# Performance work log

Measured on AMD Instinct MI355X. Metric: run time of the kernel, lower is better.

## Reference

```python
import jax, jax.numpy as jnp
import numpy as np

B = 32768        # graphs
NODES = 8        # nodes per graph (512 / 64)
N = B * NODES    # total nodes = 262144
K = 4            # Chebyshev order


def setup_inputs() -> dict:
    key = jax.random.key(0)
    ks = jax.random.split(key, 10)
    # block-diagonal fully-connected graphs (no self loops): 56 directed edges/graph
    s, d = np.nonzero(~np.eye(NODES, dtype=bool))
    offs = np.arange(B, dtype=np.int64)[:, None] * NODES
    edge_src = jnp.asarray((s[None, :] + offs).reshape(-1))
    edge_dst = jnp.asarray((d[None, :] + offs).reshape(-1))
    E = edge_src.shape[0]
    x = jax.random.normal(ks[0], (N, 8), dtype=jnp.float32)
    edge_weight = jax.random.uniform(ks[1], (E,), dtype=jnp.float32, minval=0.1, maxval=1.0)
    sc = 0.2
    return {
        'x': x, 'edge_src': edge_src, 'edge_dst': edge_dst, 'edge_weight': edge_weight,
        'w1': jax.random.normal(ks[2], (K, 8, 16), jnp.float32) * sc,  'b1': jnp.zeros((16,), jnp.float32),
        'w2': jax.random.normal(ks[3], (K, 16, 32), jnp.float32) * sc, 'b2': jnp.zeros((32,), jnp.float32),
        'w3': jax.random.normal(ks[4], (K, 32, 64), jnp.float32) * sc, 'b3': jnp.zeros((64,), jnp.float32),
        'fc1_w': jax.random.normal(ks[5], (512, 256), jnp.float32) * 0.04, 'fc1_b': jnp.zeros((256,), jnp.float32),
        'fc2_w': jax.random.normal(ks[6], (256, 128), jnp.float32) * 0.06, 'fc2_b': jnp.zeros((128,), jnp.float32),
        'fc3_w': jax.random.normal(ks[7], (128, 5), jnp.float32) * 0.09,   'fc3_b': jnp.zeros((5,), jnp.float32),
        'num_graphs': B,
    }


def _cheb(x, W, b, norm_w, edge_src, edge_dst):
    # PyG ChebConv: Tx_0 = x, Tx_1 = L_hat x, Tx_k = 2 L_hat Tx_{k-1} - Tx_{k-2}
    n = x.shape[0]
    def prop(t):  # L_hat @ t  (zero diagonal, off-diag = -D^-1/2 A D^-1/2)
        return jax.ops.segment_sum(norm_w[:, None] * t[edge_src], edge_dst, num_segments=n)
    out = x @ W[0]
    Tx0, Tx1 = x, prop(x)
    out = out + Tx1 @ W[1]
    for k in range(2, W.shape[0]):
        Tx2 = 2.0 * prop(Tx1) - Tx0
        out = out + Tx2 @ W[k]
        Tx0, Tx1 = Tx1, Tx2
    return out + b


def reference(x, edge_src, edge_dst, edge_weight, w1, b1, w2, b2, w3, b3,
              fc1_w, fc1_b, fc2_w, fc2_b, fc3_w, fc3_b, num_graphs):
    n = x.shape[0]
    # sym-normalized scaled Laplacian weights (lambda_max = 2.0)
    deg = jax.ops.segment_sum(edge_weight, edge_src, num_segments=n)
    dis = jnp.where(deg > 0, jax.lax.rsqrt(deg), 0.0)
    norm_w = -dis[edge_src] * edge_weight * dis[edge_dst]
    h = jax.nn.relu(_cheb(x, w1, b1, norm_w, edge_src, edge_dst))
    h = jax.nn.relu(_cheb(h, w2, b2, norm_w, edge_src, edge_dst))
    h = jax.nn.relu(_cheb(h, w3, b3, norm_w, edge_src, edge_dst))
    h = h.reshape(num_graphs, -1)               # (B, 512)
    h = jax.nn.relu(h @ fc1_w + fc1_b)           # dropout inactive in eval
    h = jax.nn.relu(h @ fc2_w + fc2_b)
    logits = h @ fc3_w + fc3_b
    return jax.nn.log_softmax(logits, axis=1)
```

## Files before the change

kernel.cpp:

```cpp
#include <hip/hip_runtime.h>
#include <hip/hip_bf16.h>
#include <math.h>

#define NGRAPH 32768

typedef __attribute__((ext_vector_type(8))) short short8;
typedef __attribute__((ext_vector_type(4))) float f32x4;

__device__ inline short f2bf(float f) {
    __hip_bfloat16 h = __float2bfloat16(f);
    return *reinterpret_cast<short*>(&h);
}

struct __align__(16) WaveScratch {
    float L[8][8];
    float dis[8];
    float Tt[2][32][8];
};

template<int CIN>
__device__ inline void props3(WaveScratch& S, short (*At)[136], int wid, int lane) {
    const int n = lane & 7, cb0 = lane >> 3;
#pragma unroll
    for (int k = 1; k <= 3; ++k) {
        const int pp = (k + 1) & 1;
#pragma unroll
        for (int i = 0; i < CIN / 8; ++i) {
            const int c = cb0 + 8 * i;
            float4 l0 = *(const float4*)&S.L[n][0];
            float4 l1 = *(const float4*)&S.L[n][4];
            float4 t0 = *(const float4*)&S.Tt[pp][c][0];
            float4 t1 = *(const float4*)&S.Tt[pp][c][4];
            float s = l0.x * t0.x;
            s = fmaf(l0.y, t0.y, s); s = fmaf(l0.z, t0.z, s); s = fmaf(l0.w, t0.w, s);
            s = fmaf(l1.x, t1.x, s); s = fmaf(l1.y, t1.y, s);
            s = fmaf(l1.z, t1.z, s); s = fmaf(l1.w, t1.w, s);
            float v = (k == 1) ? s : fmaf(2.f, s, -S.Tt[pp ^ 1][c][n]);
            S.Tt[pp ^ 1][c][n] = v;
            At[wid * 8 + n][k * CIN + c] = f2bf(v);
        }
    }
}

__device__ inline short8 load_bfrag(const float* __restrict__ W, int COUT, int co, int kb) {
    short8 r;
#pragma unroll
    for (int j = 0; j < 8; ++j) r[j] = f2bf(W[(size_t)(kb + j) * COUT + co]);
    return r;
}

__global__ __launch_bounds__(256, 3) void cheb_fused(
    const float* __restrict__ x,
    const float* __restrict__ ew,
    const float* __restrict__ w1, const float* __restrict__ b1,
    const float* __restrict__ w2, const float* __restrict__ b2,
    const float* __restrict__ w3, const float* __restrict__ b3,
    __hip_bfloat16* __restrict__ h3)
{
    __shared__ WaveScratch ws[4];
    __shared__ short At[32][136];
    __shared__ float sB1[16], sB2[32], sB3[64];

    const int t = threadIdx.x;
    const int wid = t >> 6, lane = t & 63;
    const int fr = lane & 15;
    const int kk = (lane >> 4) * 8;
    const int q  = lane >> 4;

    if (t < 16) sB1[t] = b1[t];
    if (t < 32) sB2[t] = b2[t];
    if (t < 64) sB3[t] = b3[t];

    short8 W1f = {};
    if (wid < 2) W1f = load_bfrag(w1, 16, fr, kk);
    short8 W2f[2];
    {
        const int nt = wid & 1;
#pragma unroll
        for (int s = 0; s < 2; ++s) W2f[s] = load_bfrag(w2, 32, nt * 16 + fr, s * 32 + kk);
    }
    short8 W3f[2][4];
    {
        const int nt0 = (wid & 1) * 2;
#pragma unroll
        for (int tt = 0; tt < 2; ++tt)
#pragma unroll
            for (int s = 0; s < 4; ++s)
                W3f[tt][s] = load_bfrag(w3, 64, (nt0 + tt) * 16 + fr, s * 32 + kk);
    }

    const int g = blockIdx.x * 4 + wid;
    WaveScratch& S = ws[wid];

    if (lane < 8) {
        const float* e = ew + (size_t)g * 56 + lane * 7;
        float d = 0.f;
#pragma unroll
        for (int j = 0; j < 7; ++j) d += e[j];
        S.dis[lane] = rsqrtf(d);
    }
    {
        float xv = x[(size_t)g * 64 + lane];
        int n = lane >> 3, c = lane & 7;
        S.Tt[0][c][n] = xv;
        At[wid * 8 + n][c] = f2bf(xv);
    }
    if (lane < 56) {
        int s = lane / 7, j = lane % 7;
        int d = j + (j >= s ? 1 : 0);
        float w = ew[(size_t)g * 56 + lane];
        S.L[d][s] = -S.dis[s] * w * S.dis[d];
    } else if (lane < 64) {
        S.L[lane - 56][lane - 56] = 0.f;
    }

    props3<8>(S, At, wid, lane);
    __syncthreads();
    if (wid < 2) {
        const int mt = wid;
        f32x4 acc = {};
        short8 a = *(const short8*)&At[mt * 16 + fr][kk];
        acc = __builtin_amdgcn_mfma_f32_16x16x32_bf16(a, W1f, acc, 0, 0, 0);
        float vr[4];
#pragma unroll
        for (int r = 0; r < 4; ++r) vr[r] = fmaxf(acc[r] + sB1[fr], 0.f);
        *(float4*)&ws[mt * 2 + (q >> 1)].Tt[0][fr][(q & 1) * 4] =
            float4{vr[0], vr[1], vr[2], vr[3]};
#pragma unroll
        for (int r = 0; r < 4; ++r) At[mt * 16 + q * 4 + r][fr] = f2bf(vr[r]);
    }
    __syncthreads();

    props3<16>(S, At, wid, lane);
    __syncthreads();
    {
        const int mt = wid >> 1, nt = wid & 1;
        f32x4 acc = {};
#pragma unroll
        for (int s = 0; s < 2; ++s) {
            short8 a = *(const short8*)&At[mt * 16 + fr][s * 32 + kk];
            acc = __builtin_amdgcn_mfma_f32_16x16x32_bf16(a, W2f[s], acc, 0, 0, 0);
        }
        const int col = nt * 16 + fr;
        float vr[4];
#pragma unroll
        for (int r = 0; r < 4; ++r) vr[r] = fmaxf(acc[r] + sB2[col], 0.f);
        *(float4*)&ws[mt * 2 + (q >> 1)].Tt[0][col][(q & 1) * 4] =
            float4{vr[0], vr[1], vr[2], vr[3]};
#pragma unroll
        for (int r = 0; r < 4; ++r) At[mt * 16 + q * 4 + r][col] = f2bf(vr[r]);
    }
    __syncthreads();

    props3<32>(S, At, wid, lane);
    __syncthreads();
    {
        const int mt = wid >> 1, nt0 = (wid & 1) * 2;
        f32x4 acc0 = {}, acc1 = {};
#pragma unroll
        for (int s = 0; s < 4; ++s) {
            short8 a = *(const short8*)&At[mt * 16 + fr][s * 32 + kk];
            acc0 = __builtin_amdgcn_mfma_f32_16x16x32_bf16(a, W3f[0][s], acc0, 0, 0, 0);
            acc1 = __builtin_amdgcn_mfma_f32_16x16x32_bf16(a, W3f[1][s], acc1, 0, 0, 0);
        }
        const int gbase = blockIdx.x * 4;
        const int c0 = nt0 * 16 + fr;
#pragma unroll
        for (int r = 0; r < 4; ++r) {
            int R = mt * 16 + q * 4 + r;
            size_t base = (size_t)(gbase + (R >> 3)) * 512 + (R & 7) * 64;
            h3[base + c0]      = __float2bfloat16(fmaxf(acc0[r] + sB3[c0], 0.f));
            h3[base + c0 + 16] = __float2bfloat16(fmaxf(acc1[r] + sB3[c0 + 16], 0.f));
        }
    }
}

__global__ __launch_bounds__(256) void transpose_cast(
    const float* __restrict__ W, __hip_bfloat16* __restrict__ Wt, int K, int N)
{
    __shared__ float tile[32][33];
    const int kb = blockIdx.x * 32, nb = blockIdx.y * 32;
    const int tx = threadIdx.x % 32, ty = threadIdx.x / 32;
    for (int i = ty; i < 32; i += 8)
        tile[i][tx] = W[(size_t)(kb + i) * N + nb + tx];
    __syncthreads();
    for (int i = ty; i < 32; i += 8)
        Wt[(size_t)(nb + i) * K + kb + tx] = __float2bfloat16(tile[tx][i]);
}

template<bool OUT_BF16>
__global__ __launch_bounds__(256) void mfma_fc(
    const __hip_bfloat16* __restrict__ A, const __hip_bfloat16* __restrict__ Bt,
    const float* __restrict__ bias, void* __restrict__ Cout, int M, int N, int K)
{
    __shared__ short As[128][40];
    __shared__ short Bs[128][40];
    const int t = threadIdx.x;
    const int wid = t >> 6, lane = t & 63;
    const int m0 = blockIdx.x * 128, n0 = blockIdx.y * 128;
    const int wm = (wid >> 1) * 64, wn = (wid & 1) * 64;

    const int r_row = t >> 1;
    const int r_k   = (t & 1) * 16;

    const int fr = lane & 15;
    const int kk = (lane >> 4) * 8;

    f32x4 acc[4][4] = {};

    for (int k0 = 0; k0 < K; k0 += 32) {
        short8 av0 = *(const short8*)&A [(size_t)(m0 + r_row) * K + k0 + r_k];
        short8 av1 = *(const short8*)&A [(size_t)(m0 + r_row) * K + k0 + r_k + 8];
        short8 bv0 = *(const short8*)&Bt[(size_t)(n0 + r_row) * K + k0 + r_k];
        short8 bv1 = *(const short8*)&Bt[(size_t)(n0 + r_row) * K + k0 + r_k + 8];
        __syncthreads();
        *(short8*)&As[r_row][r_k]     = av0;
        *(short8*)&As[r_row][r_k + 8] = av1;
        *(short8*)&Bs[r_row][r_k]     = bv0;
        *(short8*)&Bs[r_row][r_k + 8] = bv1;
        __syncthreads();

        short8 af[4], bf[4];
#pragma unroll
        for (int fm = 0; fm < 4; ++fm) af[fm] = *(const short8*)&As[wm + fm * 16 + fr][kk];
#pragma unroll
        for (int fn = 0; fn < 4; ++fn) bf[fn] = *(const short8*)&Bs[wn + fn * 16 + fr][kk];
#pragma unroll
        for (int fm = 0; fm < 4; ++fm)
#pragma unroll
            for (int fn = 0; fn < 4; ++fn)
                acc[fm][fn] = __builtin_amdgcn_mfma_f32_16x16x32_bf16(
                    af[fm], bf[fn], acc[fm][fn], 0, 0, 0);
    }

    const int orow = (lane >> 4) * 4;
#pragma unroll
    for (int fm = 0; fm < 4; ++fm) {
#pragma unroll
        for (int fn = 0; fn < 4; ++fn) {
            const int n = n0 + wn + fn * 16 + fr;
            const float bn = bias[n];
#pragma unroll
            for (int r = 0; r < 4; ++r) {
                const int m = m0 + wm + fm * 16 + orow + r;
                float v = fmaxf(acc[fm][fn][r] + bn, 0.f);
                if (OUT_BF16)
                    ((__hip_bfloat16*)Cout)[(size_t)m * N + n] = __float2bfloat16(v);
                else
                    ((float*)Cout)[(size_t)m * N + n] = v;
            }
        }
    }
}

__global__ __launch_bounds__(256) void fc3_logsoftmax(
    const float* __restrict__ A,
    const float* __restrict__ W,
    const float* __restrict__ b,
    float* __restrict__ out,
    int M)
{
    __shared__ float sW[128 * 5];
    __shared__ float sB[5];
    const int t = threadIdx.x;
    for (int i = t; i < 640; i += 256) sW[i] = W[i];
    if (t < 5) sB[t] = b[t];
    __syncthreads();

    int row = blockIdx.x * blockDim.x + t;
    if (row >= M) return;
    float logits[5];
#pragma unroll
    for (int j = 0; j < 5; ++j) logits[j] = sB[j];
    const float* a = A + (size_t)row * 128;
    for (int k = 0; k < 128; k += 4) {
        float4 av = *(const float4*)&a[k];
        const float* wk = sW + k * 5;
#pragma unroll
        for (int j = 0; j < 5; ++j) logits[j] = fmaf(av.x, wk[j], logits[j]);
#pragma unroll
        for (int j = 0; j < 5; ++j) logits[j] = fmaf(av.y, wk[5 + j], logits[j]);
#pragma unroll
        for (int j = 0; j < 5; ++j) logits[j] = fmaf(av.z, wk[10 + j], logits[j]);
#pragma unroll
        for (int j = 0; j < 5; ++j) logits[j] = fmaf(av.w, wk[15 + j], logits[j]);
    }
    float mx = logits[0];
#pragma unroll
    for (int j = 1; j < 5; ++j) mx = fmaxf(mx, logits[j]);
    float s = 0.f;
#pragma unroll
    for (int j = 0; j < 5; ++j) s += expf(logits[j] - mx);
    float lse = mx + logf(s);
#pragma unroll
    for (int j = 0; j < 5; ++j) out[(size_t)row * 5 + j] = logits[j] - lse;
}

extern "C" void kernel_launch(void* const* d_in, const int* in_sizes, int n_in,
                              void* d_out, int out_size, void* d_ws, size_t ws_size,
                              hipStream_t stream) {
    const float* x     = (const float*)d_in[0];
    const float* ew    = (const float*)d_in[3];
    const float* w1    = (const float*)d_in[4];
    const float* b1    = (const float*)d_in[5];
    const float* w2    = (const float*)d_in[6];
    const float* b2    = (const float*)d_in[7];
    const float* w3    = (const float*)d_in[8];
    const float* b3    = (const float*)d_in[9];
    const float* fc1_w = (const float*)d_in[10];
    const float* fc1_b = (const float*)d_in[11];
    const float* fc2_w = (const float*)d_in[12];
    const float* fc2_b = (const float*)d_in[13];
    const float* fc3_w = (const float*)d_in[14];
    const float* fc3_b = (const float*)d_in[15];
    float* out = (float*)d_out;

    char* p = (char*)d_ws;
    __hip_bfloat16* h3  = (__hip_bfloat16*)p;                 p += (size_t)NGRAPH * 512 * 2;
    __hip_bfloat16* a1  = (__hip_bfloat16*)p;                 p += (size_t)NGRAPH * 256 * 2;
    float*          a2  = (float*)p;                          p += (size_t)NGRAPH * 128 * 4;
    __hip_bfloat16* Wt1 = (__hip_bfloat16*)p;                 p += (size_t)256 * 512 * 2;
    __hip_bfloat16* Wt2 = (__hip_bfloat16*)p;

    transpose_cast<<<dim3(512 / 32, 256 / 32), 256, 0, stream>>>(fc1_w, Wt1, 512, 256);
    transpose_cast<<<dim3(256 / 32, 128 / 32), 256, 0, stream>>>(fc2_w, Wt2, 256, 128);
    cheb_fused<<<NGRAPH / 4, 256, 0, stream>>>(x, ew, w1, b1, w2, b2, w3, b3, h3);
    mfma_fc<true ><<<dim3(NGRAPH / 128, 256 / 128), 256, 0, stream>>>(h3, Wt1, fc1_b, a1,
                                                                      NGRAPH, 256, 512);
    mfma_fc<false><<<dim3(NGRAPH / 128, 128 / 128), 256, 0, stream>>>(a1, Wt2, fc2_b, a2,
                                                                      NGRAPH, 128, 256);
    fc3_logsoftmax<<<NGRAPH / 256, 256, 0, stream>>>(a2, fc3_w, fc3_b, out, NGRAPH);
}
```

Before: 187.1 us.

## Make Chebyshev layers wave-local, loop two graph pairs per wave, store fc2 as bf16

Each wave now handles two graphs (16 rows) end to end, with its own LDS tile, so the block-wide __syncthreads between the propagation and MFMA stages go away. Each wave holds all W1/W2/W3 fragments and biases in registers, loops twice over graph pairs, and keeps Laplacian rows in registers. Occupancy is lowered to 2 blocks per SM because of the extra register use. Separately, the fc2 output becomes bf16 to halve traffic into the fc3/log-softmax kernel, at some precision cost.

```diff
diff --git a/kernel.cpp b/kernel.cpp
--- a/kernel.cpp
+++ b/kernel.cpp
@@ -11,33 +11,36 @@
     __hip_bfloat16 h = __float2bfloat16(f);
     return *reinterpret_cast<short*>(&h);
 }
-
-struct __align__(16) WaveScratch {
-    float L[8][8];
-    float dis[8];
-    float Tt[2][32][8];
+__device__ inline float bf2f(short u) {
+    unsigned int x = ((unsigned int)(unsigned short)u) << 16;
+    return *reinterpret_cast<float*>(&x);
+}
+
+struct __align__(16) WaveCtx {
+    short At[16][136];
+    float Tt[2][32][16];
+    float L[2][8][8];
+    float dis[2][8];
 };
 
 template<int CIN>
-__device__ inline void props3(WaveScratch& S, short (*At)[136], int wid, int lane) {
-    const int n = lane & 7, cb0 = lane >> 3;
+__device__ inline void props3(WaveCtx& C, float4 Lr0, float4 Lr1,
+                              int pg, int pn, int pcb) {
 #pragma unroll
     for (int k = 1; k <= 3; ++k) {
         const int pp = (k + 1) & 1;
 #pragma unroll
-        for (int i = 0; i < CIN / 8; ++i) {
-            const int c = cb0 + 8 * i;
-            float4 l0 = *(const float4*)&S.L[n][0];
-            float4 l1 = *(const float4*)&S.L[n][4];
-            float4 t0 = *(const float4*)&S.Tt[pp][c][0];
-            float4 t1 = *(const float4*)&S.Tt[pp][c][4];
-            float s = l0.x * t0.x;
-            s = fmaf(l0.y, t0.y, s); s = fmaf(l0.z, t0.z, s); s = fmaf(l0.w, t0.w, s);
-            s = fmaf(l1.x, t1.x, s); s = fmaf(l1.y, t1.y, s);
-            s = fmaf(l1.z, t1.z, s); s = fmaf(l1.w, t1.w, s);
-            float v = (k == 1) ? s : fmaf(2.f, s, -S.Tt[pp ^ 1][c][n]);
-            S.Tt[pp ^ 1][c][n] = v;
-            At[wid * 8 + n][k * CIN + c] = f2bf(v);
+        for (int i = 0; i < CIN / 4; ++i) {
+            const int c = pcb + 4 * i;
+            float4 t0 = *(const float4*)&C.Tt[pp][c][pg * 8];
+            float4 t1 = *(const float4*)&C.Tt[pp][c][pg * 8 + 4];
+            float s = Lr0.x * t0.x;
+            s = fmaf(Lr0.y, t0.y, s); s = fmaf(Lr0.z, t0.z, s); s = fmaf(Lr0.w, t0.w, s);
+            s = fmaf(Lr1.x, t1.x, s); s = fmaf(Lr1.y, t1.y, s);
+            s = fmaf(Lr1.z, t1.z, s); s = fmaf(Lr1.w, t1.w, s);
+            float v = (k == 1) ? s : fmaf(2.f, s, -C.Tt[pp ^ 1][c][pg * 8 + pn]);
+            C.Tt[pp ^ 1][c][pg * 8 + pn] = v;
+            C.At[pg * 8 + pn][k * CIN + c] = f2bf(v);
         }
     }
 }
@@ -49,7 +52,7 @@
     return r;
 }
 
-__global__ __launch_bounds__(256, 3) void cheb_fused(
+__global__ __launch_bounds__(256, 2) void cheb_fused(
     const float* __restrict__ x,
     const float* __restrict__ ew,
     const float* __restrict__ w1, const float* __restrict__ b1,
@@ -57,120 +60,123 @@
     const float* __restrict__ w3, const float* __restrict__ b3,
     __hip_bfloat16* __restrict__ h3)
 {
-    __shared__ WaveScratch ws[4];
-    __shared__ short At[32][136];
-    __shared__ float sB1[16], sB2[32], sB3[64];
+    __shared__ WaveCtx ctx[4];
 
     const int t = threadIdx.x;
     const int wid = t >> 6, lane = t & 63;
     const int fr = lane & 15;
-    const int kk = (lane >> 4) * 8;
     const int q  = lane >> 4;
-
-    if (t < 16) sB1[t] = b1[t];
-    if (t < 32) sB2[t] = b2[t];
-    if (t < 64) sB3[t] = b3[t];
-
-    short8 W1f = {};
-    if (wid < 2) W1f = load_bfrag(w1, 16, fr, kk);
-    short8 W2f[2];
-    {
-        const int nt = wid & 1;
-#pragma unroll
-        for (int s = 0; s < 2; ++s) W2f[s] = load_bfrag(w2, 32, nt * 16 + fr, s * 32 + kk);
-    }
-    short8 W3f[2][4];
-    {
-        const int nt0 = (wid & 1) * 2;
-#pragma unroll
-        for (int tt = 0; tt < 2; ++tt)
-#pragma unroll
-            for (int s = 0; s < 4; ++s)
-                W3f[tt][s] = load_bfrag(w3, 64, (nt0 + tt) * 16 + fr, s * 32 + kk);
-    }
-
-    const int g = blockIdx.x * 4 + wid;
-    WaveScratch& S = ws[wid];
-
-    if (lane < 8) {
-        const float* e = ew + (size_t)g * 56 + lane * 7;
-        float d = 0.f;
-#pragma unroll
-        for (int j = 0; j < 7; ++j) d += e[j];
-        S.dis[lane] = rsqrtf(d);
-    }
-    {
-        float xv = x[(size_t)g * 64 + lane];
-        int n = lane >> 3, c = lane & 7;
-        S.Tt[0][c][n] = xv;
-        At[wid * 8 + n][c] = f2bf(xv);
-    }
-    if (lane < 56) {
-        int s = lane / 7, j = lane % 7;
-        int d = j + (j >= s ? 1 : 0);
-        float w = ew[(size_t)g * 56 + lane];
-        S.L[d][s] = -S.dis[s] * w * S.dis[d];
-    } else if (lane < 64) {
-        S.L[lane - 56][lane - 56] = 0.f;
-    }
-
-    props3<8>(S, At, wid, lane);
-    __syncthreads();
-    if (wid < 2) {
-        const int mt = wid;
-        f32x4 acc = {};
-        short8 a = *(const short8*)&At[mt * 16 + fr][kk];
-        acc = __builtin_amdgcn_mfma_f32_16x16x32_bf16(a, W1f, acc, 0, 0, 0);
-        float vr[4];
-#pragma unroll
-        for (int r = 0; r < 4; ++r) vr[r] = fmaxf(acc[r] + sB1[fr], 0.f);
-        *(float4*)&ws[mt * 2 + (q >> 1)].Tt[0][fr][(q & 1) * 4] =
-            float4{vr[0], vr[1], vr[2], vr[3]};
-#pragma unroll
-        for (int r = 0; r < 4; ++r) At[mt * 16 + q * 4 + r][fr] = f2bf(vr[r]);
-    }
-    __syncthreads();
-
-    props3<16>(S, At, wid, lane);
-    __syncthreads();
-    {
-        const int mt = wid >> 1, nt = wid & 1;
-        f32x4 acc = {};
-#pragma unroll
-        for (int s = 0; s < 2; ++s) {
-            short8 a = *(const short8*)&At[mt * 16 + fr][s * 32 + kk];
-            acc = __builtin_amdgcn_mfma_f32_16x16x32_bf16(a, W2f[s], acc, 0, 0, 0);
-        }
-        const int col = nt * 16 + fr;
-        float vr[4];
-#pragma unroll
-        for (int r = 0; r < 4; ++r) vr[r] = fmaxf(acc[r] + sB2[col], 0.f);
-        *(float4*)&ws[mt * 2 + (q >> 1)].Tt[0][col][(q & 1) * 4] =
-            float4{vr[0], vr[1], vr[2], vr[3]};
-#pragma unroll
-        for (int r = 0; r < 4; ++r) At[mt * 16 + q * 4 + r][col] = f2bf(vr[r]);
-    }
-    __syncthreads();
-
-    props3<32>(S, At, wid, lane);
-    __syncthreads();
-    {
-        const int mt = wid >> 1, nt0 = (wid & 1) * 2;
-        f32x4 acc0 = {}, acc1 = {};
-#pragma unroll
-        for (int s = 0; s < 4; ++s) {
-            short8 a = *(const short8*)&At[mt * 16 + fr][s * 32 + kk];
-            acc0 = __builtin_amdgcn_mfma_f32_16x16x32_bf16(a, W3f[0][s], acc0, 0, 0, 0);
-            acc1 = __builtin_amdgcn_mfma_f32_16x16x32_bf16(a, W3f[1][s], acc1, 0, 0, 0);
-        }
-        const int gbase = blockIdx.x * 4;
-        const int c0 = nt0 * 16 + fr;
-#pragma unroll
-        for (int r = 0; r < 4; ++r) {
-            int R = mt * 16 + q * 4 + r;
-            size_t base = (size_t)(gbase + (R >> 3)) * 512 + (R & 7) * 64;
-            h3[base + c0]      = __float2bfloat16(fmaxf(acc0[r] + sB3[c0], 0.f));
-            h3[base + c0 + 16] = __float2bfloat16(fmaxf(acc1[r] + sB3[c0 + 16], 0.f));
+    const int kk = q * 8;
+    WaveCtx& C = ctx[wid];
+
+    const int pg = lane >> 5, pn = lane & 7, pcb = (lane >> 3) & 3;
+
+    short8 W1f = load_bfrag(w1, 16, fr, kk);
+    short8 W2f[2][2];
+#pragma unroll
+    for (int nt = 0; nt < 2; ++nt)
+#pragma unroll
+        for (int ks = 0; ks < 2; ++ks)
+            W2f[nt][ks] = load_bfrag(w2, 32, nt * 16 + fr, ks * 32 + kk);
+    short8 W3f[4][4];
+#pragma unroll
+    for (int nt = 0; nt < 4; ++nt)
+#pragma unroll
+        for (int ks = 0; ks < 4; ++ks)
+            W3f[nt][ks] = load_bfrag(w3, 64, nt * 16 + fr, ks * 32 + kk);
+    const float b1r = b1[fr];
+    float b2r[2] = {b2[fr], b2[16 + fr]};
+    float b3r[4] = {b3[fr], b3[16 + fr], b3[32 + fr], b3[48 + fr]};
+
+#pragma unroll 1
+    for (int it = 0; it < 2; ++it) {
+        const int g0 = blockIdx.x * 16 + (it * 4 + wid) * 2;
+
+        if (lane < 16) {
+            int g = lane >> 3, n = lane & 7;
+            const float* e = ew + (size_t)(g0 + g) * 56 + n * 7;
+            float d = 0.f;
+#pragma unroll
+            for (int j = 0; j < 7; ++j) d += e[j];
+            C.dis[g][n] = rsqrtf(d);
+        }
+#pragma unroll
+        for (int j = 0; j < 2; ++j) {
+            float xv = x[(size_t)g0 * 64 + j * 64 + lane];
+            int n = lane >> 3, c = lane & 7;
+            C.Tt[0][c][j * 8 + n] = xv;
+            C.At[j * 8 + n][c] = f2bf(xv);
+        }
+#pragma unroll
+        for (int j = 0; j < 2; ++j) {
+            if (lane < 56) {
+                int s = lane / 7, jj = lane % 7;
+                int d = jj + (jj >= s ? 1 : 0);
+                float w = ew[(size_t)(g0 + j) * 56 + lane];
+                C.L[j][d][s] = -C.dis[j][s] * w * C.dis[j][d];
+            } else {
+                C.L[j][lane - 56][lane - 56] = 0.f;
+            }
+        }
+        float4 Lr0 = *(const float4*)&C.L[pg][pn][0];
+        float4 Lr1 = *(const float4*)&C.L[pg][pn][4];
+
+        props3<8>(C, Lr0, Lr1, pg, pn, pcb);
+        {
+            f32x4 acc = {};
+            short8 a = *(const short8*)&C.At[fr][kk];
+            acc = __builtin_amdgcn_mfma_f32_16x16x32_bf16(a, W1f, acc, 0, 0, 0);
+#pragma unroll
+            for (int r = 0; r < 4; ++r) {
+                int R = q * 4 + r;
+                float v = fmaxf(acc[r] + b1r, 0.f);
+                C.Tt[0][fr][R] = v;
+                C.At[R][fr] = f2bf(v);
+            }
+        }
+
+        props3<16>(C, Lr0, Lr1, pg, pn, pcb);
+        {
+            f32x4 acc[2] = {};
+#pragma unroll
+            for (int ks = 0; ks < 2; ++ks) {
+                short8 a = *(const short8*)&C.At[fr][ks * 32 + kk];
+#pragma unroll
+                for (int nt = 0; nt < 2; ++nt)
+                    acc[nt] = __builtin_amdgcn_mfma_f32_16x16x32_bf16(a, W2f[nt][ks],
+                                                                      acc[nt], 0, 0, 0);
+            }
+#pragma unroll
+            for (int nt = 0; nt < 2; ++nt)
+#pragma unroll
+                for (int r = 0; r < 4; ++r) {
+                    int R = q * 4 + r, col = nt * 16 + fr;
+                    float v = fmaxf(acc[nt][r] + b2r[nt], 0.f);
+                    C.Tt[0][col][R] = v;
+                    C.At[R][col] = f2bf(v);
+                }
+        }
+
+        props3<32>(C, Lr0, Lr1, pg, pn, pcb);
+        {
+            f32x4 acc[4] = {};
+#pragma unroll
+            for (int ks = 0; ks < 4; ++ks) {
+                short8 a = *(const short8*)&C.At[fr][ks * 32 + kk];
+#pragma unroll
+                for (int nt = 0; nt < 4; ++nt)
+                    acc[nt] = __builtin_amdgcn_mfma_f32_16x16x32_bf16(a, W3f[nt][ks],
+                                                                      acc[nt], 0, 0, 0);
+            }
+#pragma unroll
+            for (int nt = 0; nt < 4; ++nt)
+#pragma unroll
+                for (int r = 0; r < 4; ++r) {
+                    int R = q * 4 + r;
+                    int g = g0 + (R >> 3), ch = nt * 16 + fr;
+                    h3[(size_t)g * 512 + (R & 7) * 64 + ch] =
+                        __float2bfloat16(fmaxf(acc[nt][r] + b3r[nt], 0.f));
+                }
         }
     }
 }
@@ -254,7 +260,7 @@
 }
 
 __global__ __launch_bounds__(256) void fc3_logsoftmax(
-    const float* __restrict__ A,
+    const __hip_bfloat16* __restrict__ A,
     const float* __restrict__ W,
     const float* __restrict__ b,
     float* __restrict__ out,
@@ -272,18 +278,16 @@
     float logits[5];
 #pragma unroll
     for (int j = 0; j < 5; ++j) logits[j] = sB[j];
-    const float* a = A + (size_t)row * 128;
-    for (int k = 0; k < 128; k += 4) {
-        float4 av = *(const float4*)&a[k];
-        const float* wk = sW + k * 5;
-#pragma unroll
-        for (int j = 0; j < 5; ++j) logits[j] = fmaf(av.x, wk[j], logits[j]);
-#pragma unroll
-        for (int j = 0; j < 5; ++j) logits[j] = fmaf(av.y, wk[5 + j], logits[j]);
-#pragma unroll
-        for (int j = 0; j < 5; ++j) logits[j] = fmaf(av.z, wk[10 + j], logits[j]);
-#pragma unroll
-        for (int j = 0; j < 5; ++j) logits[j] = fmaf(av.w, wk[15 + j], logits[j]);
+    const short* a = (const short*)A + (size_t)row * 128;
+    for (int kb = 0; kb < 128; kb += 8) {
+        short8 av = *(const short8*)&a[kb];
+#pragma unroll
+        for (int u = 0; u < 8; ++u) {
+            float f = bf2f(av[u]);
+            const float* wk = sW + (kb + u) * 5;
+#pragma unroll
+            for (int j = 0; j < 5; ++j) logits[j] = fmaf(f, wk[j], logits[j]);
+        }
     }
     float mx = logits[0];
 #pragma unroll
@@ -318,16 +322,16 @@
     char* p = (char*)d_ws;
     __hip_bfloat16* h3  = (__hip_bfloat16*)p;                 p += (size_t)NGRAPH * 512 * 2;
     __hip_bfloat16* a1  = (__hip_bfloat16*)p;                 p += (size_t)NGRAPH * 256 * 2;
-    float*          a2  = (float*)p;                          p += (size_t)NGRAPH * 128 * 4;
+    __hip_bfloat16* a2  = (__hip_bfloat16*)p;                 p += (size_t)NGRAPH * 128 * 2;
     __hip_bfloat16* Wt1 = (__hip_bfloat16*)p;                 p += (size_t)256 * 512 * 2;
     __hip_bfloat16* Wt2 = (__hip_bfloat16*)p;
 
     transpose_cast<<<dim3(512 / 32, 256 / 32), 256, 0, stream>>>(fc1_w, Wt1, 512, 256);
     transpose_cast<<<dim3(256 / 32, 128 / 32), 256, 0, stream>>>(fc2_w, Wt2, 256, 128);
-    cheb_fused<<<NGRAPH / 4, 256, 0, stream>>>(x, ew, w1, b1, w2, b2, w3, b3, h3);
-    mfma_fc<true ><<<dim3(NGRAPH / 128, 256 / 128), 256, 0, stream>>>(h3, Wt1, fc1_b, a1,
-                                                                      NGRAPH, 256, 512);
-    mfma_fc<false><<<dim3(NGRAPH / 128, 128 / 128), 256, 0, stream>>>(a1, Wt2, fc2_b, a2,
-                                                                      NGRAPH, 128, 256);
+    cheb_fused<<<NGRAPH / 16, 256, 0, stream>>>(x, ew, w1, b1, w2, b2, w3, b3, h3);
+    mfma_fc<true><<<dim3(NGRAPH / 128, 256 / 128), 256, 0, stream>>>(h3, Wt1, fc1_b, a1,
+                                                                     NGRAPH, 256, 512);
+    mfma_fc<true><<<dim3(NGRAPH / 128, 128 / 128), 256, 0, stream>>>(a1, Wt2, fc2_b, a2,
+                                                                     NGRAPH, 128, 256);
     fc3_logsoftmax<<<NGRAPH / 256, 256, 0, stream>>>(a2, fc3_w, fc3_b, out, NGRAPH);
 }
```

Measured after the change: 187.3 us. About the same (+0.1%).
